# Kernel tuning notes

Measured on AMD Instinct MI355X. Metric: run time of the kernel, lower is better.

The kernel has to match this reference:

```python
import jax, jax.numpy as jnp
import numpy as np

N = 100000   # nodes
E = 1600000  # edges
IN = 128     # in_dim
H = 128      # hidden
C = 9        # num_classes
G = 256      # graphs in batch


def setup_inputs() -> dict:
    key = jax.random.key(0)
    ks = jax.random.split(key, 24)
    w = lambda k, shp: jax.random.normal(k, shp, dtype=jnp.float32) * 0.05
    inp = {
        "x": jax.random.normal(ks[0], (N, IN), dtype=jnp.float32),
        "edge_index": jax.random.randint(ks[1], (2, E), 0, N, dtype=jnp.int32),
        "batch": jnp.sort(jax.random.randint(ks[2], (N,), 0, G, dtype=jnp.int32)),
        # GIN layer 0 MLP: Linear(IN,H) -> ReLU -> Linear(H,H)
        "l0_w1": w(ks[3], (IN, H)), "l0_b1": jnp.zeros((H,), jnp.float32),
        "l0_w2": w(ks[4], (H, H)),  "l0_b2": jnp.zeros((H,), jnp.float32),
        # GIN layer 1 MLP
        "l1_w1": w(ks[5], (H, H)), "l1_b1": jnp.zeros((H,), jnp.float32),
        "l1_w2": w(ks[6], (H, H)), "l1_b2": jnp.zeros((H,), jnp.float32),
        # GlobalAttention gate: Linear(H,1)
        "gate_w": w(ks[7], (H, 1)), "gate_b": jnp.zeros((1,), jnp.float32),
        # classification head: Linear(H,H) -> ReLU -> Linear(H,C)
        "cls_w1": w(ks[8], (H, H)), "cls_b1": jnp.zeros((H,), jnp.float32),
        "cls_w2": w(ks[9], (H, C)), "cls_b2": jnp.zeros((C,), jnp.float32),
        "reg_w1": w(ks[10], (H, H)), "reg_b1": jnp.zeros((H,), jnp.float32),
        "reg_w2": w(ks[11], (H, 1)), "reg_b2": jnp.zeros((1,), jnp.float32),
    }
    return inp


def reference(x, edge_index, batch,
              l0_w1, l0_b1, l0_w2, l0_b2,
              l1_w1, l1_b1, l1_w2, l1_b2,
              gate_w, gate_b,
              cls_w1, cls_b1, cls_w2, cls_b2,
              reg_w1, reg_b1, reg_w2, reg_b2):
    src, dst = edge_index[0], edge_index[1]

    def gin_layer(h, w1, b1, w2, b2):
        # GINConv with eps=0: (1+eps)*h + sum_{j in N(i)} h_j, then MLP, then outer ReLU
        agg = jax.ops.segment_sum(h[src], dst, num_segments=N)
        z = h + agg
        z = jax.nn.relu(z @ w1 + b1) @ w2 + b2
        return jax.nn.relu(z)

    h = gin_layer(x, l0_w1, l0_b1, l0_w2, l0_b2)
    h = gin_layer(h, l1_w1, l1_b1, l1_w2, l1_b2)

    # GlobalAttention readout: per-graph segment softmax over gate scores
    gate = (h @ gate_w + gate_b)[:, 0]                      # [N]
    m = jax.ops.segment_max(gate, batch, num_segments=G)    # [G]
    a = jnp.exp(gate - m[batch])                            # [N]
    denom = jax.ops.segment_sum(a, batch, num_segments=G)   # [G]
    wgt = a / denom[batch]                                  # [N]
    g = jax.ops.segment_sum(h * wgt[:, None], batch, num_segments=G)  # [G, H]

    cls = jax.nn.relu(g @ cls_w1 + cls_b1) @ cls_w2 + cls_b2
    reg = jax.nn.relu(g @ reg_w1 + reg_b1) @ reg_w2 + reg_b2
    return cls, reg
```

## Files before the change

kernel.cpp:

```cpp
#include <hip/hip_runtime.h>
#include <hip/hip_fp16.h>

#define N_NODES 100000
#define N_EDGES 1600000
#define HDIM    128
#define NGRAPH  256
#define NRES    8
#define PAD     64

typedef __attribute__((ext_vector_type(8))) short short8;
typedef __attribute__((ext_vector_type(8))) _Float16 half8;
typedef __attribute__((ext_vector_type(4))) float f32x4;

__device__ inline uint pkadd(uint a, uint b) {
    __half2 r = __hadd2(__builtin_bit_cast(__half2, a), __builtin_bit_cast(__half2, b));
    return __builtin_bit_cast(uint, r);
}
__device__ inline uint4 pkadd4(uint4 a, uint4 b) {
    a.x = pkadd(a.x, b.x); a.y = pkadd(a.y, b.y);
    a.z = pkadd(a.z, b.z); a.w = pkadd(a.w, b.w);
    return a;
}
__device__ inline ushort f2h(float x) { return __half_as_ushort(__float2half_rn(x)); }
__device__ inline float h2f(ushort h) { return __half2float(__ushort_as_half(h)); }

__global__ __launch_bounds__(256) void scatter_pad_kernel(
        const int* __restrict__ src, const int* __restrict__ dst,
        int* __restrict__ cnt, int* __restrict__ eadj, int E) {
    int res  = blockIdx.x & (NRES - 1);
    int grp  = blockIdx.x >> 3;
    int ngrp = gridDim.x >> 3;
    int lo = res * (N_NODES / NRES), hi = lo + (N_NODES / NRES);
    for (int e = grp * 256 + threadIdx.x; e < E; e += ngrp * 256) {
        int d = dst[e];
        if (d >= lo && d < hi) {
            int p = atomicAdd(&cnt[d], 1);
            if (p < PAD) eadj[d * PAD + p] = src[e];
        }
    }
}

__global__ __launch_bounds__(256) void f2h_kernel(const float* __restrict__ x,
                                                  ushort* __restrict__ xh, int n4) {
    for (int i = blockIdx.x * 256 + threadIdx.x; i < n4; i += gridDim.x * 256) {
        float4 v = ((const float4*)x)[i];
        ushort4 o;
        o.x = f2h(v.x); o.y = f2h(v.y); o.z = f2h(v.z); o.w = f2h(v.w);
        ((ushort4*)xh)[i] = o;
    }
}

__global__ void pack4_kernel(const float* __restrict__ wa, const float* __restrict__ wb,
                             const float* __restrict__ wc, const float* __restrict__ wd,
                             ushort* __restrict__ ha, ushort* __restrict__ la,
                             ushort* __restrict__ hb, ushort* __restrict__ lb,
                             ushort* __restrict__ hc, ushort* __restrict__ lc,
                             ushort* __restrict__ hd, ushort* __restrict__ ld) {
    int sel = blockIdx.x >> 6;
    const float* w = sel == 0 ? wa : sel == 1 ? wb : sel == 2 ? wc : wd;
    ushort* hi = sel == 0 ? ha : sel == 1 ? hb : sel == 2 ? hc : hd;
    ushort* lo = sel == 0 ? la : sel == 1 ? lb : sel == 2 ? lc : ld;
    int t = (blockIdx.x & 63) * 256 + threadIdx.x;
    int i = t & 7, lane = (t >> 3) & 63, cfg = (t >> 9) & 7, ks = t >> 12;
    int k = ks * 32 + (lane >> 4) * 8 + i;
    int c = cfg * 16 + (lane & 15);
    float v = w[k * 128 + c];
    ushort h = f2h(v);
    hi[t] = h;
    lo[t] = f2h(v - h2f(h));
}

template<bool LAST>
__global__ __launch_bounds__(256, 6) void gin_layer_kernel(
        const ushort* __restrict__ hin,
        const int* __restrict__ cnt, const int* __restrict__ eadj,
        const ushort* __restrict__ w1h, const ushort* __restrict__ w1l,
        const float* __restrict__ b1,
        const ushort* __restrict__ w2h, const ushort* __restrict__ w2l,
        const float* __restrict__ b2,
        ushort* __restrict__ hout,
        const float* __restrict__ gw, const float* __restrict__ gb,
        float* __restrict__ gateb) {
    __shared__ ushort zt[32 * 128];
    __shared__ ushort tt[32 * 128];
    int tid  = threadIdx.x;
    int lane = tid & 63;
    int wv   = tid >> 6;
    int wvs  = __builtin_amdgcn_readfirstlane(wv);
    int row0 = blockIdx.x * 32;
    int cfg0 = wvs * 2;
    int g    = lane >> 4;
    int q    = lane & 15;
    const uint4* h4 = (const uint4*)hin;

    int baseRow = row0 + wvs * 8;
    int al[8], dg[8];
    #pragma unroll
    for (int j = 0; j < 8; j++) {
        int d = cnt[baseRow + j];
        dg[j] = d > PAD ? PAD : d;
    }
    #pragma unroll
    for (int j = 0; j < 8; j++)
        al[j] = (lane < dg[j]) ? eadj[(baseRow + j) * PAD + lane] : 0;

    uint4 acc[8];
    #pragma unroll
    for (int j = 0; j < 8; j++) {
        acc[j] = make_uint4(0u, 0u, 0u, 0u);
        if (g == 0) acc[j] = h4[(size_t)(baseRow + j) * 16 + q];
    }

    int nmax = dg[0];
    #pragma unroll
    for (int j = 1; j < 8; j++) nmax = dg[j] > nmax ? dg[j] : nmax;
    for (int c4 = 0; c4 < nmax; c4 += 4) {
        int jj = c4 + g;
        #pragma unroll
        for (int j = 0; j < 8; j++) {
            int nb = __shfl(al[j], jj);
            if (jj < dg[j]) acc[j] = pkadd4(acc[j], h4[(size_t)nb * 16 + q]);
        }
    }

    #pragma unroll
    for (int j = 0; j < 8; j++) {
        #pragma unroll
        for (int off = 16; off <= 32; off <<= 1) {
            acc[j].x = pkadd(acc[j].x, (uint)__shfl_xor((int)acc[j].x, off));
            acc[j].y = pkadd(acc[j].y, (uint)__shfl_xor((int)acc[j].y, off));
            acc[j].z = pkadd(acc[j].z, (uint)__shfl_xor((int)acc[j].z, off));
            acc[j].w = pkadd(acc[j].w, (uint)__shfl_xor((int)acc[j].w, off));
        }
        if (g == 0) {
            int lr = wvs * 8 + j;
            *(uint4*)((char*)zt + ((lr * 256 + q * 16) ^ ((lr & 7) << 4))) = acc[j];
        }
    }
    __syncthreads();

    f32x4 macc[2][2];
    #pragma unroll
    for (int rf = 0; rf < 2; rf++)
        #pragma unroll
        for (int cf = 0; cf < 2; cf++) macc[rf][cf] = (f32x4){0.f, 0.f, 0.f, 0.f};

    for (int ks = 0; ks < 4; ks++) {
        half8 bh[2], bl[2];
        #pragma unroll
        for (int cf = 0; cf < 2; cf++) {
            int bidx = (((ks * 8 + cfg0 + cf) * 64 + lane) * 8);
            bh[cf] = __builtin_bit_cast(half8, *(const short8*)&w1h[bidx]);
            bl[cf] = __builtin_bit_cast(half8, *(const short8*)&w1l[bidx]);
        }
        #pragma unroll
        for (int rf = 0; rf < 2; rf++) {
            int r = rf * 16 + q;
            int off = (r * 256 + ks * 64 + g * 16) ^ ((r & 7) << 4);
            half8 a = __builtin_bit_cast(half8, *(const short8*)((const char*)zt + off));
            #pragma unroll
            for (int cf = 0; cf < 2; cf++) {
                macc[rf][cf] = __builtin_amdgcn_mfma_f32_16x16x32_f16(a, bh[cf], macc[rf][cf], 0, 0, 0);
                macc[rf][cf] = __builtin_amdgcn_mfma_f32_16x16x32_f16(a, bl[cf], macc[rf][cf], 0, 0, 0);
            }
        }
    }

    #pragma unroll
    for (int cf = 0; cf < 2; cf++) {
        int c = (cfg0 + cf) * 16 + q;
        float bias = b1[c];
        #pragma unroll
        for (int rf = 0; rf < 2; rf++) {
            #pragma unroll
            for (int i = 0; i < 4; i++) {
                int r = rf * 16 + g * 4 + i;
                float v = fmaxf(macc[rf][cf][i] + bias, 0.f);
                int off = (r * 256 + c * 2) ^ ((r & 7) << 4);
                *(ushort*)((char*)tt + off) = f2h(v);
            }
        }
    }
    __syncthreads();

    #pragma unroll
    for (int rf = 0; rf < 2; rf++)
        #pragma unroll
        for (int cf = 0; cf < 2; cf++) macc[rf][cf] = (f32x4){0.f, 0.f, 0.f, 0.f};

    for (int ks = 0; ks < 4; ks++) {
        half8 bh[2], bl[2];
        #pragma unroll
        for (int cf = 0; cf < 2; cf++) {
            int bidx = (((ks * 8 + cfg0 + cf) * 64 + lane) * 8);
            bh[cf] = __builtin_bit_cast(half8, *(const short8*)&w2h[bidx]);
            bl[cf] = __builtin_bit_cast(half8, *(const short8*)&w2l[bidx]);
        }
        #pragma unroll
        for (int rf = 0; rf < 2; rf++) {
            int r = rf * 16 + q;
            int off = (r * 256 + ks * 64 + g * 16) ^ ((r & 7) << 4);
            half8 a = __builtin_bit_cast(half8, *(const short8*)((const char*)tt + off));
            #pragma unroll
            for (int cf = 0; cf < 2; cf++) {
                macc[rf][cf] = __builtin_amdgcn_mfma_f32_16x16x32_f16(a, bh[cf], macc[rf][cf], 0, 0, 0);
                macc[rf][cf] = __builtin_amdgcn_mfma_f32_16x16x32_f16(a, bl[cf], macc[rf][cf], 0, 0, 0);
            }
        }
    }

    float pg[8];
    if (LAST) {
        #pragma unroll
        for (int p = 0; p < 8; p++) pg[p] = 0.f;
    }
    #pragma unroll
    for (int cf = 0; cf < 2; cf++) {
        int c = (cfg0 + cf) * 16 + q;
        float bias = b2[c];
        float gwc = LAST ? gw[c] : 0.f;
        #pragma unroll
        for (int rf = 0; rf < 2; rf++) {
            #pragma unroll
            for (int i = 0; i < 4; i++) {
                int r = rf * 16 + g * 4 + i;
                float v = fmaxf(macc[rf][cf][i] + bias, 0.f);
                int off = (r * 256 + c * 2) ^ ((r & 7) << 4);
                *(ushort*)((char*)zt + off) = f2h(v);
                if (LAST) pg[rf * 4 + i] += v * gwc;
            }
        }
    }
    __syncthreads();

    #pragma unroll
    for (int p = 0; p < 2; p++) {
        int idx = tid + 256 * p;
        int r = idx >> 4, ch = idx & 15;
        uint4 v = *(const uint4*)((const char*)zt + ((r * 256 + ch * 16) ^ ((r & 7) << 4)));
        ((uint4*)hout)[(size_t)(row0 + r) * 16 + ch] = v;
    }

    if (LAST) {
        #pragma unroll
        for (int off = 1; off < 16; off <<= 1)
            #pragma unroll
            for (int p = 0; p < 8; p++) pg[p] += __shfl_xor(pg[p], off);
        float* gpart = (float*)tt;
        if (q == 0) {
            #pragma unroll
            for (int rf = 0; rf < 2; rf++)
                #pragma unroll
                for (int i = 0; i < 4; i++)
                    gpart[wvs * 32 + rf * 16 + g * 4 + i] = pg[rf * 4 + i];
        }
        __syncthreads();
        if (tid < 32) {
            gateb[row0 + tid] = gpart[tid] + gpart[32 + tid] + gpart[64 + tid]
                              + gpart[96 + tid] + gb[0];
        }
    }
}

__device__ inline int lower_bound_i(const int* a, int n, int v) {
    int lo = 0, hi = n;
    while (lo < hi) {
        int mid = (lo + hi) >> 1;
        if (a[mid] < v) lo = mid + 1; else hi = mid;
    }
    return lo;
}

__global__ __launch_bounds__(512) void readout_kernel(
        const ushort* __restrict__ h2h, const float* __restrict__ gate,
        const int* __restrict__ batch,
        const float* __restrict__ cw1, const float* __restrict__ cb1,
        const float* __restrict__ cw2, const float* __restrict__ cb2,
        const float* __restrict__ rw1, const float* __restrict__ rb1,
        const float* __restrict__ rw2, const float* __restrict__ rb2,
        float* __restrict__ out) {
    int g = blockIdx.x, t = threadIdx.x;
    int wv = t >> 6, lane = t & 63;
    __shared__ int   bounds[2];
    __shared__ float red[512];
    __shared__ float part[8][128];
    __shared__ float gv[128];
    __shared__ float t1c[128], t1r[128];
    if (t == 0) {
        bounds[0] = lower_bound_i(batch, N_NODES, g);
        bounds[1] = lower_bound_i(batch, N_NODES, g + 1);
    }
    __syncthreads();
    int s = bounds[0], e = bounds[1];

    float m = -3.4e38f;
    for (int i = s + t; i < e; i += 512) m = fmaxf(m, gate[i]);
    red[t] = m;
    __syncthreads();
    for (int off = 256; off; off >>= 1) {
        if (t < off) red[t] = fmaxf(red[t], red[t + off]);
        __syncthreads();
    }
    m = red[0];
    __syncthreads();

    float dsum = 0.f;
    for (int i = s + t; i < e; i += 512) dsum += expf(gate[i] - m);
    red[t] = dsum;
    __syncthreads();
    for (int off = 256; off; off >>= 1) {
        if (t < off) red[t] += red[t + off];
        __syncthreads();
    }
    float denom = red[0];
    float invd = (e > s && denom > 0.f) ? 1.f / denom : 0.f;

    const uint* h2u = (const uint*)h2h;
    float a0 = 0.f, a1 = 0.f, b0 = 0.f, b1v = 0.f;
    int i0 = s + wv;
    for (; i0 + 8 < e; i0 += 16) {
        float w0 = expf(gate[i0] - m);
        float w1 = expf(gate[i0 + 8] - m);
        __half2 v0 = __builtin_bit_cast(__half2, h2u[(size_t)i0 * 64 + lane]);
        __half2 v1 = __builtin_bit_cast(__half2, h2u[(size_t)(i0 + 8) * 64 + lane]);
        a0 += w0 * __low2float(v0); a1 += w0 * __high2float(v0);
        b0 += w1 * __low2float(v1); b1v += w1 * __high2float(v1);
    }
    if (i0 < e) {
        float w0 = expf(gate[i0] - m);
        __half2 v0 = __builtin_bit_cast(__half2, h2u[(size_t)i0 * 64 + lane]);
        a0 += w0 * __low2float(v0); a1 += w0 * __high2float(v0);
    }
    part[wv][lane * 2]     = a0 + b0;
    part[wv][lane * 2 + 1] = a1 + b1v;
    __syncthreads();
    if (t < 128) {
        float acc = 0.f;
        #pragma unroll
        for (int w = 0; w < 8; w++) acc += part[w][t];
        gv[t] = acc * invd;
    }
    __syncthreads();

    if (t < 128) {
        float a = cb1[t];
        for (int k = 0; k < HDIM; k++) a += gv[k] * cw1[k * HDIM + t];
        t1c[t] = fmaxf(a, 0.f);
    } else if (t < 256) {
        int tf = t - 128;
        float a = rb1[tf];
        for (int k = 0; k < HDIM; k++) a += gv[k] * rw1[k * HDIM + tf];
        t1r[tf] = fmaxf(a, 0.f);
    }
    __syncthreads();

    if (t < 9) {
        float acc2 = cb2[t];
        for (int k = 0; k < HDIM; k++) acc2 += t1c[k] * cw2[k * 9 + t];
        out[g * 9 + t] = acc2;
    }
    if (t == 64) {
        float acc2 = rb2[0];
        for (int k = 0; k < HDIM; k++) acc2 += t1r[k] * rw2[k];
        out[NGRAPH * 9 + g] = acc2;
    }
}

extern "C" void kernel_launch(void* const* d_in, const int* in_sizes, int n_in,
                              void* d_out, int out_size, void* d_ws, size_t ws_size,
                              hipStream_t stream) {
    const float* x     = (const float*)d_in[0];
    const int*   ei    = (const int*)d_in[1];
    const int*   batch = (const int*)d_in[2];
    const float *l0w1 = (const float*)d_in[3],  *l0b1 = (const float*)d_in[4];
    const float *l0w2 = (const float*)d_in[5],  *l0b2 = (const float*)d_in[6];
    const float *l1w1 = (const float*)d_in[7],  *l1b1 = (const float*)d_in[8];
    const float *l1w2 = (const float*)d_in[9],  *l1b2 = (const float*)d_in[10];
    const float *gw   = (const float*)d_in[11], *gb   = (const float*)d_in[12];
    const float *cw1  = (const float*)d_in[13], *cb1  = (const float*)d_in[14];
    const float *cw2  = (const float*)d_in[15], *cb2  = (const float*)d_in[16];
    const float *rw1  = (const float*)d_in[17], *rb1  = (const float*)d_in[18];
    const float *rw2  = (const float*)d_in[19], *rb2  = (const float*)d_in[20];
    const int* src = ei;
    const int* dst = ei + N_EDGES;
    float* out = (float*)d_out;

    char* ws = (char*)d_ws;
    size_t o = 0;
    auto alloc = [&](size_t bytes) { void* p = ws + o; o = (o + bytes + 255) & ~(size_t)255; return p; };
    ushort* h2h   = (ushort*)alloc((size_t)N_NODES * HDIM * 2);
    ushort* xh    = h2h;
    ushort* h1h   = (ushort*)alloc((size_t)N_NODES * HDIM * 2);
    int*    eadj  = (int*)alloc((size_t)N_NODES * PAD * 4);
    int*    cnt   = (int*)alloc(N_NODES * 4);
    float*  gateb = (float*)alloc(N_NODES * 4);
    ushort* w0h1 = (ushort*)alloc(16384 * 2), *w0l1 = (ushort*)alloc(16384 * 2);
    ushort* w0h2 = (ushort*)alloc(16384 * 2), *w0l2 = (ushort*)alloc(16384 * 2);
    ushort* w1h1 = (ushort*)alloc(16384 * 2), *w1l1 = (ushort*)alloc(16384 * 2);
    ushort* w1h2 = (ushort*)alloc(16384 * 2), *w1l2 = (ushort*)alloc(16384 * 2);
    (void)ws_size; (void)in_sizes; (void)n_in; (void)out_size;

    pack4_kernel<<<256, 256, 0, stream>>>(l0w1, l0w2, l1w1, l1w2,
                                          w0h1, w0l1, w0h2, w0l2,
                                          w1h1, w1l1, w1h2, w1l2);

    hipMemsetAsync(cnt, 0, N_NODES * 4, stream);
    scatter_pad_kernel<<<2048, 256, 0, stream>>>(src, dst, cnt, eadj, N_EDGES);
    f2h_kernel<<<1024, 256, 0, stream>>>(x, xh, N_NODES * HDIM / 4);

    const int layerBlocks = N_NODES / 32;
    gin_layer_kernel<false><<<layerBlocks, 256, 0, stream>>>(
        xh, cnt, eadj, w0h1, w0l1, l0b1, w0h2, w0l2, l0b2,
        h1h, gw, gb, nullptr);
    gin_layer_kernel<true><<<layerBlocks, 256, 0, stream>>>(
        h1h, cnt, eadj, w1h1, w1l1, l1b1, w1h2, w1l2, l1b2,
        h2h, gw, gb, gateb);

    readout_kernel<<<NGRAPH, 512, 0, stream>>>(h2h, gateb, batch,
                                               cw1, cb1, cw2, cb2,
                                               rw1, rb1, rw2, rb2, out);
}
```

Measured before the change: 294.8 us.

## Fuse weight pack with x conversion, vectorize scatter, widen readout, raise occupancy

Merges the weight-packing and x-to-fp16 conversion kernels into a single launch, which removes one kernel launch. The edge scatter now reads dst as int4, so each thread handles four edges. The GIN layer's launch-bounds occupancy hint goes from 6 to 8 blocks, which may force register spills. The readout uses 1024 threads per graph with 16 warps. Several unrelated changes are bundled together.

New measurement: 288.9 us. 1.02x faster.

```diff
diff --git a/kernel.cpp b/kernel.cpp
--- a/kernel.cpp
+++ b/kernel.cpp
@@ -26,52 +26,56 @@
 
 __global__ __launch_bounds__(256) void scatter_pad_kernel(
         const int* __restrict__ src, const int* __restrict__ dst,
-        int* __restrict__ cnt, int* __restrict__ eadj, int E) {
+        int* __restrict__ cnt, int* __restrict__ eadj, int E4) {
     int res  = blockIdx.x & (NRES - 1);
     int grp  = blockIdx.x >> 3;
     int ngrp = gridDim.x >> 3;
     int lo = res * (N_NODES / NRES), hi = lo + (N_NODES / NRES);
-    for (int e = grp * 256 + threadIdx.x; e < E; e += ngrp * 256) {
-        int d = dst[e];
-        if (d >= lo && d < hi) {
-            int p = atomicAdd(&cnt[d], 1);
-            if (p < PAD) eadj[d * PAD + p] = src[e];
-        }
-    }
-}
-
-__global__ __launch_bounds__(256) void f2h_kernel(const float* __restrict__ x,
-                                                  ushort* __restrict__ xh, int n4) {
-    for (int i = blockIdx.x * 256 + threadIdx.x; i < n4; i += gridDim.x * 256) {
-        float4 v = ((const float4*)x)[i];
-        ushort4 o;
-        o.x = f2h(v.x); o.y = f2h(v.y); o.z = f2h(v.z); o.w = f2h(v.w);
-        ((ushort4*)xh)[i] = o;
-    }
-}
-
-__global__ void pack4_kernel(const float* __restrict__ wa, const float* __restrict__ wb,
-                             const float* __restrict__ wc, const float* __restrict__ wd,
-                             ushort* __restrict__ ha, ushort* __restrict__ la,
-                             ushort* __restrict__ hb, ushort* __restrict__ lb,
-                             ushort* __restrict__ hc, ushort* __restrict__ lc,
-                             ushort* __restrict__ hd, ushort* __restrict__ ld) {
-    int sel = blockIdx.x >> 6;
-    const float* w = sel == 0 ? wa : sel == 1 ? wb : sel == 2 ? wc : wd;
-    ushort* hi = sel == 0 ? ha : sel == 1 ? hb : sel == 2 ? hc : hd;
-    ushort* lo = sel == 0 ? la : sel == 1 ? lb : sel == 2 ? lc : ld;
-    int t = (blockIdx.x & 63) * 256 + threadIdx.x;
-    int i = t & 7, lane = (t >> 3) & 63, cfg = (t >> 9) & 7, ks = t >> 12;
-    int k = ks * 32 + (lane >> 4) * 8 + i;
-    int c = cfg * 16 + (lane & 15);
-    float v = w[k * 128 + c];
-    ushort h = f2h(v);
-    hi[t] = h;
-    lo[t] = f2h(v - h2f(h));
+    const int4* dst4 = (const int4*)dst;
+    for (int e4 = grp * 256 + threadIdx.x; e4 < E4; e4 += ngrp * 256) {
+        int4 d = dst4[e4];
+        int e = e4 * 4;
+        if (d.x >= lo && d.x < hi) { int p = atomicAdd(&cnt[d.x], 1); if (p < PAD) eadj[d.x * PAD + p] = src[e]; }
+        if (d.y >= lo && d.y < hi) { int p = atomicAdd(&cnt[d.y], 1); if (p < PAD) eadj[d.y * PAD + p] = src[e + 1]; }
+        if (d.z >= lo && d.z < hi) { int p = atomicAdd(&cnt[d.z], 1); if (p < PAD) eadj[d.z * PAD + p] = src[e + 2]; }
+        if (d.w >= lo && d.w < hi) { int p = atomicAdd(&cnt[d.w], 1); if (p < PAD) eadj[d.w * PAD + p] = src[e + 3]; }
+    }
+}
+
+__global__ void prep_kernel(const float* __restrict__ wa, const float* __restrict__ wb,
+                            const float* __restrict__ wc, const float* __restrict__ wd,
+                            ushort* __restrict__ ha, ushort* __restrict__ la,
+                            ushort* __restrict__ hb, ushort* __restrict__ lb,
+                            ushort* __restrict__ hc, ushort* __restrict__ lc,
+                            ushort* __restrict__ hd, ushort* __restrict__ ld,
+                            const float* __restrict__ x, ushort* __restrict__ xh, int n4) {
+    int bid = blockIdx.x;
+    if (bid < 256) {
+        int sel = bid >> 6;
+        const float* w = sel == 0 ? wa : sel == 1 ? wb : sel == 2 ? wc : wd;
+        ushort* hi = sel == 0 ? ha : sel == 1 ? hb : sel == 2 ? hc : hd;
+        ushort* lo = sel == 0 ? la : sel == 1 ? lb : sel == 2 ? lc : ld;
+        int t = (bid & 63) * 256 + threadIdx.x;
+        int i = t & 7, lane = (t >> 3) & 63, cfg = (t >> 9) & 7, ks = t >> 12;
+        int k = ks * 32 + (lane >> 4) * 8 + i;
+        int c = cfg * 16 + (lane & 15);
+        float v = w[k * 128 + c];
+        ushort h = f2h(v);
+        hi[t] = h;
+        lo[t] = f2h(v - h2f(h));
+    } else {
+        int nb = gridDim.x - 256;
+        for (int i = (bid - 256) * 256 + threadIdx.x; i < n4; i += nb * 256) {
+            float4 v = ((const float4*)x)[i];
+            ushort4 o;
+            o.x = f2h(v.x); o.y = f2h(v.y); o.z = f2h(v.z); o.w = f2h(v.w);
+            ((ushort4*)xh)[i] = o;
+        }
+    }
 }
 
 template<bool LAST>
-__global__ __launch_bounds__(256, 6) void gin_layer_kernel(
+__global__ __launch_bounds__(256, 8) void gin_layer_kernel(
         const ushort* __restrict__ hin,
         const int* __restrict__ cnt, const int* __restrict__ eadj,
         const ushort* __restrict__ w1h, const ushort* __restrict__ w1l,
@@ -271,7 +275,7 @@
     return lo;
 }
 
-__global__ __launch_bounds__(512) void readout_kernel(
+__global__ __launch_bounds__(1024) void readout_kernel(
         const ushort* __restrict__ h2h, const float* __restrict__ gate,
         const int* __restrict__ batch,
         const float* __restrict__ cw1, const float* __restrict__ cb1,
@@ -282,8 +286,8 @@
     int g = blockIdx.x, t = threadIdx.x;
     int wv = t >> 6, lane = t & 63;
     __shared__ int   bounds[2];
-    __shared__ float red[512];
-    __shared__ float part[8][128];
+    __shared__ float red[1024];
+    __shared__ float part[16][128];
     __shared__ float gv[128];
     __shared__ float t1c[128], t1r[128];
     if (t == 0) {
@@ -294,10 +298,10 @@
     int s = bounds[0], e = bounds[1];
 
     float m = -3.4e38f;
-    for (int i = s + t; i < e; i += 512) m = fmaxf(m, gate[i]);
+    for (int i = s + t; i < e; i += 1024) m = fmaxf(m, gate[i]);
     red[t] = m;
     __syncthreads();
-    for (int off = 256; off; off >>= 1) {
+    for (int off = 512; off; off >>= 1) {
         if (t < off) red[t] = fmaxf(red[t], red[t + off]);
         __syncthreads();
     }
@@ -305,10 +309,10 @@
     __syncthreads();
 
     float dsum = 0.f;
-    for (int i = s + t; i < e; i += 512) dsum += expf(gate[i] - m);
+    for (int i = s + t; i < e; i += 1024) dsum += expf(gate[i] - m);
     red[t] = dsum;
     __syncthreads();
-    for (int off = 256; off; off >>= 1) {
+    for (int off = 512; off; off >>= 1) {
         if (t < off) red[t] += red[t + off];
         __syncthreads();
     }
@@ -318,11 +322,11 @@
     const uint* h2u = (const uint*)h2h;
     float a0 = 0.f, a1 = 0.f, b0 = 0.f, b1v = 0.f;
     int i0 = s + wv;
-    for (; i0 + 8 < e; i0 += 16) {
+    for (; i0 + 16 < e; i0 += 32) {
         float w0 = expf(gate[i0] - m);
-        float w1 = expf(gate[i0 + 8] - m);
+        float w1 = expf(gate[i0 + 16] - m);
         __half2 v0 = __builtin_bit_cast(__half2, h2u[(size_t)i0 * 64 + lane]);
-        __half2 v1 = __builtin_bit_cast(__half2, h2u[(size_t)(i0 + 8) * 64 + lane]);
+        __half2 v1 = __builtin_bit_cast(__half2, h2u[(size_t)(i0 + 16) * 64 + lane]);
         a0 += w0 * __low2float(v0); a1 += w0 * __high2float(v0);
         b0 += w1 * __low2float(v1); b1v += w1 * __high2float(v1);
     }
@@ -337,7 +341,7 @@
     if (t < 128) {
         float acc = 0.f;
         #pragma unroll
-        for (int w = 0; w < 8; w++) acc += part[w][t];
+        for (int w = 0; w < 16; w++) acc += part[w][t];
         gv[t] = acc * invd;
     }
     __syncthreads();
@@ -400,13 +404,13 @@
     ushort* w1h2 = (ushort*)alloc(16384 * 2), *w1l2 = (ushort*)alloc(16384 * 2);
     (void)ws_size; (void)in_sizes; (void)n_in; (void)out_size;
 
-    pack4_kernel<<<256, 256, 0, stream>>>(l0w1, l0w2, l1w1, l1w2,
+    prep_kernel<<<1280, 256, 0, stream>>>(l0w1, l0w2, l1w1, l1w2,
                                           w0h1, w0l1, w0h2, w0l2,
-                                          w1h1, w1l1, w1h2, w1l2);
+                                          w1h1, w1l1, w1h2, w1l2,
+                                          x, xh, N_NODES * HDIM / 4);
 
     hipMemsetAsync(cnt, 0, N_NODES * 4, stream);
-    scatter_pad_kernel<<<2048, 256, 0, stream>>>(src, dst, cnt, eadj, N_EDGES);
-    f2h_kernel<<<1024, 256, 0, stream>>>(x, xh, N_NODES * HDIM / 4);
+    scatter_pad_kernel<<<2048, 256, 0, stream>>>(src, dst, cnt, eadj, N_EDGES / 4);
 
     const int layerBlocks = N_NODES / 32;
     gin_layer_kernel<false><<<layerBlocks, 256, 0, stream>>>(
@@ -416,7 +420,7 @@
         h1h, cnt, eadj, w1h1, w1l1, l1b1, w1h2, w1l2, l1b2,
         h2h, gw, gb, gateb);
 
-    readout_kernel<<<NGRAPH, 512, 0, stream>>>(h2h, gateb, batch,
-                                               cw1, cb1, cw2, cb2,
-                                               rw1, rb1, rw2, rb2, out);
-}
+    readout_kernel<<<NGRAPH, 1024, 0, stream>>>(h2h, gateb, batch,
+                                                cw1, cb1, cw2, cb2,
+                                                rw1, rb1, rw2, rb2, out);
+}
```
